# Kernel optimization log

Measured on AMD Instinct MI355X. Metric: run time of the kernel, lower is better.

Reference implementation:

```python
import jax, jax.numpy as jnp
import numpy as np

N_NODES = 100000
N_EDGES = 800000
HIDDEN = 128


def setup_inputs() -> dict:
    key = jax.random.key(0)
    k1, k2, k3, k4, k5, k6 = jax.random.split(key, 6)
    z = jax.random.normal(k1, (N_NODES, HIDDEN), dtype=jnp.float32)
    edge_index = jax.random.randint(k2, (2, N_EDGES), 0, N_NODES, dtype=jnp.int64)
    # nn.Linear params (torch default init scale ~ 1/sqrt(fan_in))
    s1 = 1.0 / np.sqrt(2 * HIDDEN)
    s2 = 1.0 / np.sqrt(HIDDEN)
    W1 = jax.random.uniform(k3, (2 * HIDDEN, HIDDEN), jnp.float32, -s1, s1)
    b1 = jax.random.uniform(k4, (HIDDEN,), jnp.float32, -s1, s1)
    W2 = jax.random.uniform(k5, (HIDDEN, 1), jnp.float32, -s2, s2)
    b2 = jax.random.uniform(k6, (1,), jnp.float32, -s2, s2)
    return {"z": z, "edge_index": edge_index, "W1": W1, "b1": b1, "W2": W2, "b2": b2}


def reference(z, edge_index, W1, b1, W2, b2):
    src, dst = edge_index[0], edge_index[1]
    # Gather endpoint features: [E, H] each. Avoid materializing the [E, 2H]
    # concat by splitting W1 into src/dst halves (same math as cat + matmul).
    W1_src, W1_dst = W1[:HIDDEN], W1[HIDDEN:]
    h = z[src] @ W1_src + z[dst] @ W1_dst + b1  # [E, H]
    h = jax.nn.relu(h)
    score = h @ W2 + b2  # [E, 1]
    return score
```

## Files before the change

kernel.cpp:

```cpp
#include <hip/hip_runtime.h>
#include <hip/hip_bf16.h>

#define N_NODES 100000
#define N_EDGES 800000
#define HIDDEN 128
#define N_TILES 1563
#define PC_GRID 768

typedef short frag_ab __attribute__((ext_vector_type(8)));
typedef float frag_cd __attribute__((ext_vector_type(4)));

__device__ inline unsigned short f2b(float f) {
    union { float f; unsigned u; } x; x.f = f;
    return (unsigned short)((x.u + 0x7fffu + ((x.u >> 16) & 1u)) >> 16);
}

__global__ __launch_bounds__(256) void transpose_w1(
    const float* __restrict__ W1, unsigned short* __restrict__ Bt)
{
    const int t  = threadIdx.x;
    const int nc = blockIdx.x * 4 + (t >> 6);
    const int k2 = (t & 63) * 2;
    const int col  = nc & 127;
    const int roff = (nc >= 128) ? 128 : 0;
    float f0 = W1[(size_t)(roff + k2)     * HIDDEN + col];
    float f1 = W1[(size_t)(roff + k2 + 1) * HIDDEN + col];
    unsigned pack = (unsigned)f2b(f0) | ((unsigned)f2b(f1) << 16);
    *(unsigned*)(Bt + (size_t)nc * HIDDEN + k2) = pack;
}

#define AS_STRIDE 136
#define CS_STRIDE 264

__global__ __launch_bounds__(256) void precompute_uv_mfma(
    const float* __restrict__ z, const unsigned short* __restrict__ Bt,
    const float* __restrict__ b1, unsigned short* __restrict__ UV)
{
    __shared__ unsigned short As[64 * AS_STRIDE];
    __shared__ unsigned short Cs[64 * CS_STRIDE];
    const int t = threadIdx.x;
    const int lane = t & 63;
    const int w = t >> 6;
    const int wn = w * 64;
    const int g  = lane >> 4;
    const int lc = lane & 15;

    frag_ab b[4][4];
    float bias[4];
    #pragma unroll
    for (int nt = 0; nt < 4; ++nt) {
        int nc = wn + nt * 16 + lc;
        bias[nt] = (nc < HIDDEN) ? b1[nc] : 0.f;
        const unsigned short* brow = Bt + (size_t)nc * HIDDEN;
        #pragma unroll
        for (int q = 0; q < 4; ++q)
            b[nt][q] = *(const frag_ab*)(brow + q * 32 + g * 8);
    }

    int tile = blockIdx.x;
    float4 pf[8];
    #pragma unroll
    for (int i = 0; i < 8; ++i) {
        int f4 = i * 256 + t;
        int m = tile * 64 + (f4 >> 5);
        if (m >= N_NODES) m = N_NODES - 1;
        pf[i] = ((const float4*)z)[(size_t)m * 32 + (f4 & 31)];
    }

    while (true) {
        #pragma unroll
        for (int i = 0; i < 8; ++i) {
            int f4 = i * 256 + t;
            int m = f4 >> 5;
            int c4 = f4 & 31;
            uint2 p;
            p.x = (unsigned)f2b(pf[i].x) | ((unsigned)f2b(pf[i].y) << 16);
            p.y = (unsigned)f2b(pf[i].z) | ((unsigned)f2b(pf[i].w) << 16);
            *(uint2*)&As[m * AS_STRIDE + c4 * 4] = p;
        }
        __syncthreads();

        const int next = tile + PC_GRID;
        const bool have_next = (next < N_TILES);
        if (have_next) {
            #pragma unroll
            for (int i = 0; i < 8; ++i) {
                int f4 = i * 256 + t;
                int m = next * 64 + (f4 >> 5);
                if (m >= N_NODES) m = N_NODES - 1;
                pf[i] = ((const float4*)z)[(size_t)m * 32 + (f4 & 31)];
            }
        }

        frag_cd acc[4][4];
        #pragma unroll
        for (int mt = 0; mt < 4; ++mt)
            #pragma unroll
            for (int nt = 0; nt < 4; ++nt)
                acc[mt][nt] = (frag_cd){0.f, 0.f, 0.f, 0.f};
        #pragma unroll
        for (int q = 0; q < 4; ++q) {
            frag_ab a[4];
            #pragma unroll
            for (int mt = 0; mt < 4; ++mt)
                a[mt] = *(const frag_ab*)&As[(mt * 16 + lc) * AS_STRIDE + q * 32 + g * 8];
            #pragma unroll
            for (int mt = 0; mt < 4; ++mt)
                #pragma unroll
                for (int nt = 0; nt < 4; ++nt)
                    acc[mt][nt] = __builtin_amdgcn_mfma_f32_16x16x32_bf16(
                        a[mt], b[nt][q], acc[mt][nt], 0, 0, 0);
        }
        __syncthreads();

        #pragma unroll
        for (int nt = 0; nt < 4; ++nt) {
            int nc = wn + nt * 16 + lc;
            #pragma unroll
            for (int mt = 0; mt < 4; ++mt)
                #pragma unroll
                for (int r = 0; r < 4; ++r)
                    Cs[(mt * 16 + g * 4 + r) * CS_STRIDE + nc] =
                        f2b(acc[mt][nt][r] + bias[nt]);
        }
        __syncthreads();

        const int m0 = tile * 64;
        #pragma unroll
        for (int i = 0; i < 8; ++i) {
            int f = i * 256 + t;
            int m = f >> 5;
            int c16 = f & 31;
            if (m0 + m < N_NODES) {
                uint4 val = *(const uint4*)&Cs[m * CS_STRIDE + c16 * 8];
                *(uint4*)&UV[(size_t)(m0 + m) * 256 + c16 * 8] = val;
            }
        }
        if (!have_next) break;
        __syncthreads();
        tile = next;
    }
}

__device__ inline float2 bf2(unsigned u) {
    union { unsigned i; float f; } lo, hi;
    lo.i = u << 16;
    hi.i = u & 0xffff0000u;
    return make_float2(lo.f, hi.f);
}

__device__ inline float2 rfma2(unsigned u, unsigned v, float2 w, float2 acc) {
    float2 uf = bf2(u), vf = bf2(v);
    float2 s = make_float2(uf.x + vf.x, uf.y + vf.y);
    s.x = fmaxf(s.x, 0.f); s.y = fmaxf(s.y, 0.f);
    acc.x = __builtin_fmaf(s.x, w.x, acc.x);
    acc.y = __builtin_fmaf(s.y, w.y, acc.y);
    return acc;
}

__global__ __launch_bounds__(256) void edge_score(
    const int* __restrict__ ei, const unsigned short* __restrict__ UV,
    const float* __restrict__ W2, const float* __restrict__ B2,
    float* __restrict__ out)
{
    const int t = threadIdx.x;
    const int g = t & 7;
    const int slot = t >> 3;
    const int e0 = blockIdx.x * 64 + slot;
    const int e1 = e0 + 32;

    const float4* W24 = (const float4*)W2;
    const float4 w0 = W24[g * 4 + 0];
    const float4 w1 = W24[g * 4 + 1];
    const float4 w2 = W24[g * 4 + 2];
    const float4 w3 = W24[g * 4 + 3];

    const int s0 = ei[e0];
    const int d0 = ei[N_EDGES + e0];
    const int s1 = ei[e1];
    const int d1 = ei[N_EDGES + e1];

    const uint4* u0p = (const uint4*)(UV + (size_t)s0 * 256) + g * 2;
    const uint4* v0p = (const uint4*)(UV + (size_t)d0 * 256 + 128) + g * 2;
    const uint4* u1p = (const uint4*)(UV + (size_t)s1 * 256) + g * 2;
    const uint4* v1p = (const uint4*)(UV + (size_t)d1 * 256 + 128) + g * 2;
    const uint4 ua0 = u0p[0], ub0 = u0p[1];
    const uint4 va0 = v0p[0], vb0 = v0p[1];
    const uint4 ua1 = u1p[0], ub1 = u1p[1];
    const uint4 va1 = v1p[0], vb1 = v1p[1];

    float2 A = make_float2(0.f, 0.f), B = make_float2(0.f, 0.f);
    A = rfma2(ua0.x, va0.x, make_float2(w0.x, w0.y), A);
    A = rfma2(ua0.y, va0.y, make_float2(w0.z, w0.w), A);
    A = rfma2(ua0.z, va0.z, make_float2(w1.x, w1.y), A);
    A = rfma2(ua0.w, va0.w, make_float2(w1.z, w1.w), A);
    A = rfma2(ub0.x, vb0.x, make_float2(w2.x, w2.y), A);
    A = rfma2(ub0.y, vb0.y, make_float2(w2.z, w2.w), A);
    A = rfma2(ub0.z, vb0.z, make_float2(w3.x, w3.y), A);
    A = rfma2(ub0.w, vb0.w, make_float2(w3.z, w3.w), A);

    B = rfma2(ua1.x, va1.x, make_float2(w0.x, w0.y), B);
    B = rfma2(ua1.y, va1.y, make_float2(w0.z, w0.w), B);
    B = rfma2(ua1.z, va1.z, make_float2(w1.x, w1.y), B);
    B = rfma2(ua1.w, va1.w, make_float2(w1.z, w1.w), B);
    B = rfma2(ub1.x, vb1.x, make_float2(w2.x, w2.y), B);
    B = rfma2(ub1.y, vb1.y, make_float2(w2.z, w2.w), B);
    B = rfma2(ub1.z, vb1.z, make_float2(w3.x, w3.y), B);
    B = rfma2(ub1.w, vb1.w, make_float2(w3.z, w3.w), B);

    float sa = A.x + A.y;
    float sb = B.x + B.y;
    sa += __shfl_xor(sa, 1, 8);
    sa += __shfl_xor(sa, 2, 8);
    sa += __shfl_xor(sa, 4, 8);
    sb += __shfl_xor(sb, 1, 8);
    sb += __shfl_xor(sb, 2, 8);
    sb += __shfl_xor(sb, 4, 8);

    if (g == 0) {
        float bb = B2[0];
        out[e0] = sa + bb;
        out[e1] = sb + bb;
    }
}

extern "C" void kernel_launch(void* const* d_in, const int* in_sizes, int n_in,
                              void* d_out, int out_size, void* d_ws, size_t ws_size,
                              hipStream_t stream) {
    const float* z  = (const float*)d_in[0];
    const int*   ei = (const int*)d_in[1];
    const float* W1 = (const float*)d_in[2];
    const float* b1 = (const float*)d_in[3];
    const float* W2 = (const float*)d_in[4];
    const float* b2 = (const float*)d_in[5];
    float* out = (float*)d_out;

    unsigned short* UV = (unsigned short*)d_ws;
    unsigned short* Bt = UV + (size_t)N_NODES * 256;

    transpose_w1<<<64, 256, 0, stream>>>(W1, Bt);
    precompute_uv_mfma<<<PC_GRID, 256, 0, stream>>>(z, Bt, b1, UV);
    edge_score<<<N_EDGES / 64, 256, 0, stream>>>(ei, UV, W2, b2, out);
}
```

Measured before the change: 166.0 us.

## Alias LDS buffers, pack prefetch to bf16 early, raise precompute grid occupancy

The precompute kernel now shares one LDS buffer between the A tile and the output staging tile, which is safe because a barrier separates the two uses. This cuts shared memory per block so more blocks can be resident, and launch bounds now ask for 3 blocks per SM. Prefetched z values are converted to packed bf16 right after loading using the HIP intrinsic, which halves the prefetch registers. The persistent grid grows from 768 to 1024 blocks. The risk is that converting right after the load may stall on load latency instead of letting the load overlap with the MFMA work.

```diff
diff --git a/kernel.cpp b/kernel.cpp
--- a/kernel.cpp
+++ b/kernel.cpp
@@ -5,7 +5,7 @@
 #define N_EDGES 800000
 #define HIDDEN 128
 #define N_TILES 1563
-#define PC_GRID 768
+#define PC_GRID 1024
 
 typedef short frag_ab __attribute__((ext_vector_type(8)));
 typedef float frag_cd __attribute__((ext_vector_type(4)));
@@ -13,6 +13,12 @@
 __device__ inline unsigned short f2b(float f) {
     union { float f; unsigned u; } x; x.f = f;
     return (unsigned short)((x.u + 0x7fffu + ((x.u >> 16) & 1u)) >> 16);
+}
+
+__device__ inline unsigned pk2(float x, float y) {
+    union { __hip_bfloat162 h; unsigned u; } c;
+    c.h = __float22bfloat162_rn(make_float2(x, y));
+    return c.u;
 }
 
 __global__ __launch_bounds__(256) void transpose_w1(
@@ -25,19 +31,17 @@
     const int roff = (nc >= 128) ? 128 : 0;
     float f0 = W1[(size_t)(roff + k2)     * HIDDEN + col];
     float f1 = W1[(size_t)(roff + k2 + 1) * HIDDEN + col];
-    unsigned pack = (unsigned)f2b(f0) | ((unsigned)f2b(f1) << 16);
-    *(unsigned*)(Bt + (size_t)nc * HIDDEN + k2) = pack;
+    *(unsigned*)(Bt + (size_t)nc * HIDDEN + k2) = (unsigned)f2b(f0) | ((unsigned)f2b(f1) << 16);
 }
 
 #define AS_STRIDE 136
 #define CS_STRIDE 264
 
-__global__ __launch_bounds__(256) void precompute_uv_mfma(
+__global__ __launch_bounds__(256, 3) void precompute_uv_mfma(
     const float* __restrict__ z, const unsigned short* __restrict__ Bt,
     const float* __restrict__ b1, unsigned short* __restrict__ UV)
 {
-    __shared__ unsigned short As[64 * AS_STRIDE];
-    __shared__ unsigned short Cs[64 * CS_STRIDE];
+    __shared__ unsigned short smem[64 * CS_STRIDE];
     const int t = threadIdx.x;
     const int lane = t & 63;
     const int w = t >> 6;
@@ -58,25 +62,22 @@
     }
 
     int tile = blockIdx.x;
-    float4 pf[8];
+    uint2 pf[8];
     #pragma unroll
     for (int i = 0; i < 8; ++i) {
         int f4 = i * 256 + t;
         int m = tile * 64 + (f4 >> 5);
         if (m >= N_NODES) m = N_NODES - 1;
-        pf[i] = ((const float4*)z)[(size_t)m * 32 + (f4 & 31)];
+        float4 v = ((const float4*)z)[(size_t)m * 32 + (f4 & 31)];
+        pf[i].x = pk2(v.x, v.y);
+        pf[i].y = pk2(v.z, v.w);
     }
 
     while (true) {
         #pragma unroll
         for (int i = 0; i < 8; ++i) {
             int f4 = i * 256 + t;
-            int m = f4 >> 5;
-            int c4 = f4 & 31;
-            uint2 p;
-            p.x = (unsigned)f2b(pf[i].x) | ((unsigned)f2b(pf[i].y) << 16);
-            p.y = (unsigned)f2b(pf[i].z) | ((unsigned)f2b(pf[i].w) << 16);
-            *(uint2*)&As[m * AS_STRIDE + c4 * 4] = p;
+            *(uint2*)&smem[(f4 >> 5) * AS_STRIDE + (f4 & 31) * 4] = pf[i];
         }
         __syncthreads();
 
@@ -88,7 +89,9 @@
                 int f4 = i * 256 + t;
                 int m = next * 64 + (f4 >> 5);
                 if (m >= N_NODES) m = N_NODES - 1;
-                pf[i] = ((const float4*)z)[(size_t)m * 32 + (f4 & 31)];
+                float4 v = ((const float4*)z)[(size_t)m * 32 + (f4 & 31)];
+                pf[i].x = pk2(v.x, v.y);
+                pf[i].y = pk2(v.z, v.w);
             }
         }
 
@@ -103,7 +106,7 @@
             frag_ab a[4];
             #pragma unroll
             for (int mt = 0; mt < 4; ++mt)
-                a[mt] = *(const frag_ab*)&As[(mt * 16 + lc) * AS_STRIDE + q * 32 + g * 8];
+                a[mt] = *(const frag_ab*)&smem[(mt * 16 + lc) * AS_STRIDE + q * 32 + g * 8];
             #pragma unroll
             for (int mt = 0; mt < 4; ++mt)
                 #pragma unroll
@@ -120,7 +123,7 @@
             for (int mt = 0; mt < 4; ++mt)
                 #pragma unroll
                 for (int r = 0; r < 4; ++r)
-                    Cs[(mt * 16 + g * 4 + r) * CS_STRIDE + nc] =
+                    smem[(mt * 16 + g * 4 + r) * CS_STRIDE + nc] =
                         f2b(acc[mt][nt][r] + bias[nt]);
         }
         __syncthreads();
@@ -132,7 +135,7 @@
             int m = f >> 5;
             int c16 = f & 31;
             if (m0 + m < N_NODES) {
-                uint4 val = *(const uint4*)&Cs[m * CS_STRIDE + c16 * 8];
+                uint4 val = *(const uint4*)&smem[m * CS_STRIDE + c16 * 8];
                 *(uint4*)&UV[(size_t)(m0 + m) * 256 + c16 * 8] = val;
             }
         }
```

Result: slower. 194.4 us (+17.1%).
